# Optimization experiments

Hardware: AMD Instinct MI355X
Metric: run time of the kernel (lower is better)

Reference implementation:

```python
import jax, jax.numpy as jnp
import numpy as np

B = 32768
HID = 64
IU = np.triu_indices(9)  # 45 upper-triangular (incl. diagonal) entries of a 9x9 matrix
DIAG = np.arange(9)


def setup_inputs() -> dict:
    key = jax.random.key(0)
    ks = jax.random.split(key, 12)
    return {
        "x": jax.random.normal(ks[0], (B, 1, 9, 7), jnp.float32),
        "adj": jax.random.randint(ks[1], (B, 45), 0, 2, jnp.int32),
        "context": jax.random.normal(ks[2], (B, 1, 9, 5), jnp.float32),
        # DenseGCNConv(7, 7): linear weight + bias
        "gcn_W": jax.random.normal(ks[3], (7, 7), jnp.float32) * 0.3,
        "gcn_b": jax.random.normal(ks[4], (7,), jnp.float32) * 0.05,
        # context_net Linear(45, 63)
        "ctx_W": jax.random.normal(ks[5], (45, 63), jnp.float32) * 0.15,
        "ctx_b": jax.random.normal(ks[6], (63,), jnp.float32) * 0.05,
        # three 1x1 convs: 2->64, 64->64, 64->2 (weights stored [out, in])
        "W1": jax.random.normal(ks[7], (HID, 2), jnp.float32) * 0.5,
        "b1": jnp.zeros((HID,), jnp.float32),
        "W2": jax.random.normal(ks[8], (HID, HID), jnp.float32) * 0.12,
        "b2": jnp.zeros((HID,), jnp.float32),
        "W3": jax.random.normal(ks[9], (2, HID), jnp.float32) * 0.12,
        "b3": jnp.zeros((2,), jnp.float32),
    }


def reference(x, adj, context, gcn_W, gcn_b, ctx_W, ctx_b, W1, b1, W2, b2, W3, b3):
    Bn = x.shape[0]
    # scatter 45 edge values into the upper triangle of a [B,9,9] adjacency, binarize
    A = jnp.zeros((Bn, 9, 9), jnp.float32).at[:, IU[0], IU[1]].set(adj.astype(jnp.float32))
    A = (A > 0.0).astype(jnp.float32)
    # DenseGCNConv: add self-loops (diag := 1), symmetric degree normalization
    A = A.at[:, DIAG, DIAG].set(1.0)
    d = jnp.maximum(A.sum(-1), 1.0) ** -0.5  # [B,9]
    An = d[:, :, None] * A * d[:, None, :]
    z = x[:, 0]  # [B,9,7]
    z = jnp.einsum('bnm,bmf->bnf', An, z @ gcn_W) + gcn_b  # [B,9,7]
    # context MLP: flatten -> Linear(45,63) -> ReLU -> reshape (9,7)
    c = jax.nn.relu(context.reshape(Bn, 1, 45) @ ctx_W + ctx_b).reshape(Bn, 1, 9, 7)
    h = jnp.concatenate([z[:, None], c], axis=1)  # [B,2,9,7]
    # 1x1 conv stack == per-pixel channel GEMMs
    h = jax.nn.relu(jnp.einsum('bchw,oc->bohw', h, W1) + b1[:, None, None])
    h = jax.nn.relu(jnp.einsum('bchw,oc->bohw', h, W2) + b2[:, None, None])
    return jnp.einsum('bchw,oc->bohw', h, W3) + b3[:, None, None]  # [B,2,9,7]
```

## Files before the change

### kernel.cpp

```cpp
#include <hip/hip_runtime.h>
#include <cstdint>

#define BLOCK_SIZE 256
#define NPOS 63

typedef __attribute__((ext_vector_type(8))) short bf16x8;
typedef __attribute__((ext_vector_type(4))) float f32x4;
typedef __attribute__((ext_vector_type(4))) unsigned int uint4v;

template <int CTRL>
__device__ __forceinline__ float dpp_add(float v) {
    const int m = __builtin_amdgcn_update_dpp(0, __float_as_int(v), CTRL, 0xF, 0xF, true);
    return v + __int_as_float(m);
}
__device__ __forceinline__ float row16_sum(float v) {
    v = dpp_add<0xB1>(v);
    v = dpp_add<0x4E>(v);
    v = dpp_add<0x124>(v);
    v = dpp_add<0x128>(v);
    return v;
}

__device__ __forceinline__ unsigned pack_hi16(float ha, float hb) {
    return __builtin_amdgcn_perm(__float_as_uint(hb), __float_as_uint(ha), 0x07060302u);
}

__global__ __launch_bounds__(256) void w2split_kernel(
    const float* __restrict__ W2, short* __restrict__ w2h, short* __restrict__ w2l)
{
    const int i = blockIdx.x * 256 + threadIdx.x;
    if (i < 4096) {
        const float w = W2[i];
        const unsigned u = __float_as_uint(w);
        w2h[i] = (short)(u >> 16);
        const float l = w - __uint_as_float(u & 0xFFFF0000u);
        w2l[i] = (short)(__float_as_uint(l) >> 16);
    }
}

__global__ __launch_bounds__(BLOCK_SIZE) void carnet_zc(
    const float* __restrict__ x,
    const int*   __restrict__ adj,
    const float* __restrict__ ctx,
    const float* __restrict__ gcn_W,
    const float* __restrict__ gcn_b,
    const float* __restrict__ ctx_W,
    const float* __restrict__ ctx_b,
    float2* __restrict__ zcbuf)
{
    const int t    = threadIdx.x;
    const int lane = t & 63;
    const int b    = __builtin_amdgcn_readfirstlane(blockIdx.x * 4 + (t >> 6));

    const int p = lane < 63 ? lane : 62;
    const int n = p / 7;
    const int f = p - n * 7;

    const int* ab = adj + b * 45;
    uint64_t am = 0;
#pragma unroll
    for (int i = 0; i < 45; ++i)
        am |= (uint64_t)(ab[i] != 0) << i;

    float d[9];
#pragma unroll
    for (int i = 0; i < 9; ++i) {
        const int s = 9 * i - (i * (i - 1)) / 2;
        const int w = 8 - i;
        const uint64_t bits = (am >> (s + 1)) & ((1ull << w) - 1ull);
        d[i] = __frsqrt_rn((float)(1 + __popcll(bits)));
    }

    const float* xb = x + b * 63;
    float yv = 0.f;
#pragma unroll
    for (int k = 0; k < 7; ++k)
        yv = fmaf(xb[n * 7 + k], gcn_W[k * 7 + f], yv);

    float zt = 0.f;
    const int snn = 9 * n - (n * (n - 1)) / 2 - n;
#pragma unroll
    for (int m = 0; m < 9; ++m) {
        const float ym = __shfl(yv, m * 7 + f);
        int sh = snn + m;
        sh = sh < 0 ? 0 : sh;
        const bool conn = (m == n) || ((m > n) && ((am >> sh) & 1ull));
        zt = fmaf(conn ? d[m] : 0.f, ym, zt);
    }
    const float zv = fmaf(d[n], zt, gcn_b[f]);

    const float* cb = ctx + b * 45;
    float cacc = ctx_b[p];
#pragma unroll
    for (int q = 0; q < 45; ++q)
        cacc = fmaf(cb[q], ctx_W[q * 63 + p], cacc);
    const float cvv = fmaxf(cacc, 0.f);

    if (lane < 63)
        zcbuf[b * 63 + lane] = make_float2(zv, cvv);
}

__global__ __launch_bounds__(BLOCK_SIZE) void carnet_mfma(
    const float2* __restrict__ zcbuf,
    const float* __restrict__ W1,
    const float* __restrict__ b1,
    const short* __restrict__ w2h,
    const short* __restrict__ w2l,
    const float* __restrict__ b2,
    const float* __restrict__ W3,
    const float* __restrict__ b3,
    float* __restrict__ out)
{
    __shared__ short sh2h[64 * 64];
    __shared__ short sh2l[64 * 64];

    const int t    = threadIdx.x;
    const int lane = t & 63;
    const int b    = __builtin_amdgcn_readfirstlane(blockIdx.x * 4 + (t >> 6));

#pragma unroll
    for (int j0 = 0; j0 < 2; ++j0) {
        const int j = j0 * 256 + t;
        const int r = j >> 3, c = j & 7;
        const int slot = c ^ (r & 7);
        *(uint4v*)&sh2h[r * 64 + slot * 8] = ((const uint4v*)w2h)[j];
        *(uint4v*)&sh2l[r * 64 + slot * 8] = ((const uint4v*)w2l)[j];
    }

    const int pl = lane < 63 ? lane : 62;
    const float2 zc = zcbuf[b * 63 + pl];
    const float zv = zc.x, cvv = zc.y;

    const int cl   = lane & 15;
    const int quad = lane >> 4;
    const int s0 = (quad ^ (cl & 7)) * 16;

    float2 wp0[8], wp1[8];
    float  bb0[8], bb1[8];
#pragma unroll
    for (int j = 0; j < 8; ++j) {
        const int o = quad * 8 + j;
        wp0[j] = *(const float2*)(W1 + 2 * o);
        bb0[j] = b1[o];
        wp1[j] = *(const float2*)(W1 + 2 * (o + 32));
        bb1[j] = b1[o + 32];
    }

    const float b2v0 = b2[cl],      b2v1 = b2[16 + cl];
    const float b2v2 = b2[32 + cl], b2v3 = b2[48 + cl];
    const float w3a0 = W3[cl],      w3a1 = W3[16 + cl];
    const float w3a2 = W3[32 + cl], w3a3 = W3[48 + cl];
    const float w3b0 = W3[64 + cl], w3b1 = W3[80 + cl];
    const float w3b2 = W3[96 + cl], w3b3 = W3[112 + cl];
    const float b30 = b3[0], b31 = b3[1];
    float* __restrict__ ob = out + b * 126;

    const char* sh2hB = (const char*)sh2h;
    const char* sh2lB = (const char*)sh2l;

    __syncthreads();

#pragma unroll 1
    for (int i = 0; i < 4; ++i) {
        const float zm = __shfl(zv,  i * 16 + cl);
        const float cm = __shfl(cvv, i * 16 + cl);

        uint4v ph0, pl0, ph1, pl1;
#pragma unroll
        for (int jj = 0; jj < 4; ++jj) {
            float ha = fmaxf(fmaf(wp0[2*jj].x,   zm, fmaf(wp0[2*jj].y,   cm, bb0[2*jj])),   0.f);
            float hb = fmaxf(fmaf(wp0[2*jj+1].x, zm, fmaf(wp0[2*jj+1].y, cm, bb0[2*jj+1])), 0.f);
            ph0[jj] = pack_hi16(ha, hb);
            float la = ha - __uint_as_float(__float_as_uint(ha) & 0xFFFF0000u);
            float lb = hb - __uint_as_float(__float_as_uint(hb) & 0xFFFF0000u);
            pl0[jj] = pack_hi16(la, lb);

            ha = fmaxf(fmaf(wp1[2*jj].x,   zm, fmaf(wp1[2*jj].y,   cm, bb1[2*jj])),   0.f);
            hb = fmaxf(fmaf(wp1[2*jj+1].x, zm, fmaf(wp1[2*jj+1].y, cm, bb1[2*jj+1])), 0.f);
            ph1[jj] = pack_hi16(ha, hb);
            la = ha - __uint_as_float(__float_as_uint(ha) & 0xFFFF0000u);
            lb = hb - __uint_as_float(__float_as_uint(hb) & 0xFFFF0000u);
            pl1[jj] = pack_hi16(la, lb);
        }
        const bf16x8 ah0 = __builtin_bit_cast(bf16x8, ph0);
        const bf16x8 al0 = __builtin_bit_cast(bf16x8, pl0);
        const bf16x8 ah1 = __builtin_bit_cast(bf16x8, ph1);
        const bf16x8 al1 = __builtin_bit_cast(bf16x8, pl1);

        f32x4 acc0 = {b2v0, b2v0, b2v0, b2v0};
        f32x4 acc1 = {b2v1, b2v1, b2v1, b2v1};
        f32x4 acc2 = {b2v2, b2v2, b2v2, b2v2};
        f32x4 acc3 = {b2v3, b2v3, b2v3, b2v3};

#define STEP(nt) {                                                                    \
        int bo = cl * 128 + s0;                                                       \
        asm volatile("" : "+v"(bo));                                                  \
        const int bo2 = (cl * 128) | (s0 ^ 64);                                       \
        const bf16x8 bh0 = *(const bf16x8*)(sh2hB + bo  + ((nt) * 2048));             \
        const bf16x8 bh1 = *(const bf16x8*)(sh2hB + bo2 + ((nt) * 2048));             \
        const bf16x8 bl0 = *(const bf16x8*)(sh2lB + bo  + ((nt) * 2048));             \
        const bf16x8 bl1 = *(const bf16x8*)(sh2lB + bo2 + ((nt) * 2048));             \
        acc##nt = __builtin_amdgcn_mfma_f32_16x16x32_bf16(ah0, bh0, acc##nt, 0, 0, 0); \
        acc##nt = __builtin_amdgcn_mfma_f32_16x16x32_bf16(al0, bh0, acc##nt, 0, 0, 0); \
        acc##nt = __builtin_amdgcn_mfma_f32_16x16x32_bf16(ah0, bl0, acc##nt, 0, 0, 0); \
        acc##nt = __builtin_amdgcn_mfma_f32_16x16x32_bf16(ah1, bh1, acc##nt, 0, 0, 0); \
        acc##nt = __builtin_amdgcn_mfma_f32_16x16x32_bf16(al1, bh1, acc##nt, 0, 0, 0); \
        acc##nt = __builtin_amdgcn_mfma_f32_16x16x32_bf16(ah1, bl1, acc##nt, 0, 0, 0); }
        STEP(0) STEP(1) STEP(2) STEP(3)
#undef STEP

        const int ppBase = i * 16 + quad * 4;
#define REDST(reg) {                                                          \
        const float h20 = fmaxf(acc0[reg], 0.f);                              \
        const float h21 = fmaxf(acc1[reg], 0.f);                              \
        const float h22 = fmaxf(acc2[reg], 0.f);                              \
        const float h23 = fmaxf(acc3[reg], 0.f);                              \
        float q0 = fmaf(h23, w3a3, fmaf(h22, w3a2, fmaf(h21, w3a1, h20 * w3a0))); \
        float q1 = fmaf(h23, w3b3, fmaf(h22, w3b2, fmaf(h21, w3b1, h20 * w3b0))); \
        q0 = row16_sum(q0);                                                   \
        q1 = row16_sum(q1);                                                   \
        const int pp = ppBase + (reg);                                        \
        if (cl == 0 && pp < NPOS) {                                           \
            ob[pp]        = q0 + b30;                                         \
            ob[NPOS + pp] = q1 + b31;                                         \
        } }
        REDST(0) REDST(1) REDST(2) REDST(3)
#undef REDST
    }
}

extern "C" void kernel_launch(void* const* d_in, const int* in_sizes, int n_in,
                              void* d_out, int out_size, void* d_ws, size_t ws_size,
                              hipStream_t stream) {
    const float* x     = (const float*)d_in[0];
    const int*   adj   = (const int*)  d_in[1];
    const float* ctx   = (const float*)d_in[2];
    const float* gcn_W = (const float*)d_in[3];
    const float* gcn_b = (const float*)d_in[4];
    const float* ctx_W = (const float*)d_in[5];
    const float* ctx_b = (const float*)d_in[6];
    const float* W1    = (const float*)d_in[7];
    const float* b1    = (const float*)d_in[8];
    const float* W2    = (const float*)d_in[9];
    const float* b2    = (const float*)d_in[10];
    const float* W3    = (const float*)d_in[11];
    const float* b3    = (const float*)d_in[12];
    float* out = (float*)d_out;

    short* w2h = (short*)d_ws;
    short* w2l = w2h + 4096;

    w2split_kernel<<<16, 256, 0, stream>>>(W2, w2h, w2l);

    const int nbatch = in_sizes[1] / 45;
    const int grid = (nbatch + 3) / 4;

    carnet_zc<<<grid, BLOCK_SIZE, 0, stream>>>(
        x, adj, ctx, gcn_W, gcn_b, ctx_W, ctx_b, (float2*)out);

    carnet_mfma<<<grid, BLOCK_SIZE, 0, stream>>>(
        (const float2*)out, W1, b1, w2h, w2l, b2, W3, b3, out);
}
```

Baseline: 179.3 us.

## Fuse GCN/context stage, W2 split and MFMA stack into one kernel

Merges the three launches (W2 hi/lo bf16 split, GCN+context MLP producing z/c, and the MFMA conv stack) into a single kernel. Each block now converts W2 to hi/lo bf16 directly from fp32 while staging it into swizzled LDS, and computes z and c in registers instead of writing and re-reading them through the output buffer. This removes two kernel launches and a global round trip of the intermediate, at the cost of redundant per-block W2 conversion and higher register pressure in the fused kernel.

```diff
diff --git a/kernel.cpp b/kernel.cpp
--- a/kernel.cpp
+++ b/kernel.cpp
@@ -24,21 +24,11 @@
 __device__ __forceinline__ unsigned pack_hi16(float ha, float hb) {
     return __builtin_amdgcn_perm(__float_as_uint(hb), __float_as_uint(ha), 0x07060302u);
 }
-
-__global__ __launch_bounds__(256) void w2split_kernel(
-    const float* __restrict__ W2, short* __restrict__ w2h, short* __restrict__ w2l)
-{
-    const int i = blockIdx.x * 256 + threadIdx.x;
-    if (i < 4096) {
-        const float w = W2[i];
-        const unsigned u = __float_as_uint(w);
-        w2h[i] = (short)(u >> 16);
-        const float l = w - __uint_as_float(u & 0xFFFF0000u);
-        w2l[i] = (short)(__float_as_uint(l) >> 16);
-    }
-}
-
-__global__ __launch_bounds__(BLOCK_SIZE) void carnet_zc(
+__device__ __forceinline__ float lo_part(float h) {
+    return h - __uint_as_float(__float_as_uint(h) & 0xFFFF0000u);
+}
+
+__global__ __launch_bounds__(BLOCK_SIZE) void carnet_fused(
     const float* __restrict__ x,
     const int*   __restrict__ adj,
     const float* __restrict__ ctx,
@@ -46,66 +36,9 @@
     const float* __restrict__ gcn_b,
     const float* __restrict__ ctx_W,
     const float* __restrict__ ctx_b,
-    float2* __restrict__ zcbuf)
-{
-    const int t    = threadIdx.x;
-    const int lane = t & 63;
-    const int b    = __builtin_amdgcn_readfirstlane(blockIdx.x * 4 + (t >> 6));
-
-    const int p = lane < 63 ? lane : 62;
-    const int n = p / 7;
-    const int f = p - n * 7;
-
-    const int* ab = adj + b * 45;
-    uint64_t am = 0;
-#pragma unroll
-    for (int i = 0; i < 45; ++i)
-        am |= (uint64_t)(ab[i] != 0) << i;
-
-    float d[9];
-#pragma unroll
-    for (int i = 0; i < 9; ++i) {
-        const int s = 9 * i - (i * (i - 1)) / 2;
-        const int w = 8 - i;
-        const uint64_t bits = (am >> (s + 1)) & ((1ull << w) - 1ull);
-        d[i] = __frsqrt_rn((float)(1 + __popcll(bits)));
-    }
-
-    const float* xb = x + b * 63;
-    float yv = 0.f;
-#pragma unroll
-    for (int k = 0; k < 7; ++k)
-        yv = fmaf(xb[n * 7 + k], gcn_W[k * 7 + f], yv);
-
-    float zt = 0.f;
-    const int snn = 9 * n - (n * (n - 1)) / 2 - n;
-#pragma unroll
-    for (int m = 0; m < 9; ++m) {
-        const float ym = __shfl(yv, m * 7 + f);
-        int sh = snn + m;
-        sh = sh < 0 ? 0 : sh;
-        const bool conn = (m == n) || ((m > n) && ((am >> sh) & 1ull));
-        zt = fmaf(conn ? d[m] : 0.f, ym, zt);
-    }
-    const float zv = fmaf(d[n], zt, gcn_b[f]);
-
-    const float* cb = ctx + b * 45;
-    float cacc = ctx_b[p];
-#pragma unroll
-    for (int q = 0; q < 45; ++q)
-        cacc = fmaf(cb[q], ctx_W[q * 63 + p], cacc);
-    const float cvv = fmaxf(cacc, 0.f);
-
-    if (lane < 63)
-        zcbuf[b * 63 + lane] = make_float2(zv, cvv);
-}
-
-__global__ __launch_bounds__(BLOCK_SIZE) void carnet_mfma(
-    const float2* __restrict__ zcbuf,
     const float* __restrict__ W1,
     const float* __restrict__ b1,
-    const short* __restrict__ w2h,
-    const short* __restrict__ w2l,
+    const float* __restrict__ W2,
     const float* __restrict__ b2,
     const float* __restrict__ W3,
     const float* __restrict__ b3,
@@ -116,20 +49,79 @@
 
     const int t    = threadIdx.x;
     const int lane = t & 63;
-    const int b    = __builtin_amdgcn_readfirstlane(blockIdx.x * 4 + (t >> 6));
-
-#pragma unroll
-    for (int j0 = 0; j0 < 2; ++j0) {
-        const int j = j0 * 256 + t;
-        const int r = j >> 3, c = j & 7;
-        const int slot = c ^ (r & 7);
-        *(uint4v*)&sh2h[r * 64 + slot * 8] = ((const uint4v*)w2h)[j];
-        *(uint4v*)&sh2l[r * 64 + slot * 8] = ((const uint4v*)w2l)[j];
-    }
-
-    const int pl = lane < 63 ? lane : 62;
-    const float2 zc = zcbuf[b * 63 + pl];
-    const float zv = zc.x, cvv = zc.y;
+
+    {
+        const int r  = t >> 2;
+        const int cq = t & 3;
+        const float* wsrc = W2 + r * 64 + cq * 16;
+        const float4 w0 = ((const float4*)wsrc)[0];
+        const float4 w1 = ((const float4*)wsrc)[1];
+        const float4 w2v = ((const float4*)wsrc)[2];
+        const float4 w3v = ((const float4*)wsrc)[3];
+        uint4v hA = { pack_hi16(w0.x, w0.y),  pack_hi16(w0.z, w0.w),
+                      pack_hi16(w1.x, w1.y),  pack_hi16(w1.z, w1.w) };
+        uint4v hB = { pack_hi16(w2v.x, w2v.y), pack_hi16(w2v.z, w2v.w),
+                      pack_hi16(w3v.x, w3v.y), pack_hi16(w3v.z, w3v.w) };
+        uint4v lA = { pack_hi16(lo_part(w0.x), lo_part(w0.y)),
+                      pack_hi16(lo_part(w0.z), lo_part(w0.w)),
+                      pack_hi16(lo_part(w1.x), lo_part(w1.y)),
+                      pack_hi16(lo_part(w1.z), lo_part(w1.w)) };
+        uint4v lB = { pack_hi16(lo_part(w2v.x), lo_part(w2v.y)),
+                      pack_hi16(lo_part(w2v.z), lo_part(w2v.w)),
+                      pack_hi16(lo_part(w3v.x), lo_part(w3v.y)),
+                      pack_hi16(lo_part(w3v.z), lo_part(w3v.w)) };
+        const int sA = ((2 * cq)     ^ (r & 7)) * 8;
+        const int sB = ((2 * cq + 1) ^ (r & 7)) * 8;
+        *(uint4v*)&sh2h[r * 64 + sA] = hA;
+        *(uint4v*)&sh2h[r * 64 + sB] = hB;
+        *(uint4v*)&sh2l[r * 64 + sA] = lA;
+        *(uint4v*)&sh2l[r * 64 + sB] = lB;
+    }
+
+    const int b = __builtin_amdgcn_readfirstlane(blockIdx.x * 4 + (t >> 6));
+    const int p = lane < 63 ? lane : 62;
+    const int n = p / 7;
+    const int f = p - n * 7;
+
+    const int* ab = adj + b * 45;
+    uint64_t am = 0;
+#pragma unroll
+    for (int i = 0; i < 45; ++i)
+        am |= (uint64_t)(ab[i] != 0) << i;
+
+    float d[9];
+#pragma unroll
+    for (int i = 0; i < 9; ++i) {
+        const int s = 9 * i - (i * (i - 1)) / 2;
+        const int w = 8 - i;
+        const uint64_t bits = (am >> (s + 1)) & ((1ull << w) - 1ull);
+        d[i] = __frsqrt_rn((float)(1 + __popcll(bits)));
+    }
+
+    const float* xb = x + b * 63;
+    float yv = 0.f;
+#pragma unroll
+    for (int k = 0; k < 7; ++k)
+        yv = fmaf(xb[n * 7 + k], gcn_W[k * 7 + f], yv);
+
+    float zt = 0.f;
+    const int snn = 9 * n - (n * (n - 1)) / 2 - n;
+#pragma unroll
+    for (int m = 0; m < 9; ++m) {
+        const float ym = __shfl(yv, m * 7 + f);
+        int sh = snn + m;
+        sh = sh < 0 ? 0 : sh;
+        const bool conn = (m == n) || ((m > n) && ((am >> sh) & 1ull));
+        zt = fmaf(conn ? d[m] : 0.f, ym, zt);
+    }
+    const float zv = fmaf(d[n], zt, gcn_b[f]);
+
+    const float* cb = ctx + b * 45;
+    float cacc = ctx_b[p];
+#pragma unroll
+    for (int q = 0; q < 45; ++q)
+        cacc = fmaf(cb[q], ctx_W[q * 63 + p], cacc);
+    const float cvv = fmaxf(cacc, 0.f);
 
     const int cl   = lane & 15;
     const int quad = lane >> 4;
@@ -171,16 +163,12 @@
             float ha = fmaxf(fmaf(wp0[2*jj].x,   zm, fmaf(wp0[2*jj].y,   cm, bb0[2*jj])),   0.f);
             float hb = fmaxf(fmaf(wp0[2*jj+1].x, zm, fmaf(wp0[2*jj+1].y, cm, bb0[2*jj+1])), 0.f);
             ph0[jj] = pack_hi16(ha, hb);
-            float la = ha - __uint_as_float(__float_as_uint(ha) & 0xFFFF0000u);
-            float lb = hb - __uint_as_float(__float_as_uint(hb) & 0xFFFF0000u);
-            pl0[jj] = pack_hi16(la, lb);
+            pl0[jj] = pack_hi16(lo_part(ha), lo_part(hb));
 
             ha = fmaxf(fmaf(wp1[2*jj].x,   zm, fmaf(wp1[2*jj].y,   cm, bb1[2*jj])),   0.f);
             hb = fmaxf(fmaf(wp1[2*jj+1].x, zm, fmaf(wp1[2*jj+1].y, cm, bb1[2*jj+1])), 0.f);
             ph1[jj] = pack_hi16(ha, hb);
-            la = ha - __uint_as_float(__float_as_uint(ha) & 0xFFFF0000u);
-            lb = hb - __uint_as_float(__float_as_uint(hb) & 0xFFFF0000u);
-            pl1[jj] = pack_hi16(la, lb);
+            pl1[jj] = pack_hi16(lo_part(ha), lo_part(hb));
         }
         const bf16x8 ah0 = __builtin_bit_cast(bf16x8, ph0);
         const bf16x8 al0 = __builtin_bit_cast(bf16x8, pl0);
@@ -247,17 +235,9 @@
     const float* b3    = (const float*)d_in[12];
     float* out = (float*)d_out;
 
-    short* w2h = (short*)d_ws;
-    short* w2l = w2h + 4096;
-
-    w2split_kernel<<<16, 256, 0, stream>>>(W2, w2h, w2l);
-
     const int nbatch = in_sizes[1] / 45;
     const int grid = (nbatch + 3) / 4;
-
-    carnet_zc<<<grid, BLOCK_SIZE, 0, stream>>>(
-        x, adj, ctx, gcn_W, gcn_b, ctx_W, ctx_b, (float2*)out);
-
-    carnet_mfma<<<grid, BLOCK_SIZE, 0, stream>>>(
-        (const float2*)out, W1, b1, w2h, w2l, b2, W3, b3, out);
-}
+    carnet_fused<<<grid, BLOCK_SIZE, 0, stream>>>(
+        x, adj, ctx, gcn_W, gcn_b, ctx_W, ctx_b,
+        W1, b1, W2, b2, W3, b3, out);
+}
```

Measured after the change: 183.1 us. 2.1% more time.
